# Kernel tuning notes

Measured on AMD Instinct MI355X. Metric: run time of the kernel, lower is better.

The kernel has to match this reference:

```python
import jax, jax.numpy as jnp
import numpy as np

NC = 10          # num_clusters
D_MODEL = 512
H = 8
DK = 64          # d_model = H*DK
B = 8
L = 2048


def _mlp2(x, W1, b1, W2, b2):
    h = jax.nn.gelu(x @ W1 + b1, approximate=False)
    return h @ W2 + b2


def setup_inputs() -> dict:
    key = jax.random.key(0)
    ks = jax.random.split(key, 12)
    s_in = 1.0 / np.sqrt(D_MODEL)
    s_h = 1.0 / np.sqrt(4 * NC)
    s_nc = 1.0 / np.sqrt(NC)
    return {
        "Q": jax.random.normal(ks[0], (B, H, L, DK), jnp.float32),
        "K": jax.random.normal(ks[1], (B, H, L, DK), jnp.float32),
        "V": jax.random.normal(ks[2], (B, H, L, DK), jnp.float32),
        # cluster_k_proj: Linear(d_model,4*nc) GELU Linear(4*nc,nc); stored as [in,out]
        "Wk1": jax.random.normal(ks[3], (D_MODEL, 4 * NC), jnp.float32) * s_in,
        "bk1": jnp.zeros((4 * NC,), jnp.float32),
        "Wk2": jax.random.normal(ks[4], (4 * NC, NC), jnp.float32) * s_h,
        "bk2": jnp.zeros((NC,), jnp.float32),
        # cluster_q_proj
        "Wq1": jax.random.normal(ks[5], (D_MODEL, 4 * NC), jnp.float32) * s_in,
        "bq1": jnp.zeros((4 * NC,), jnp.float32),
        "Wq2": jax.random.normal(ks[6], (4 * NC, NC), jnp.float32) * s_h,
        "bq2": jnp.zeros((NC,), jnp.float32),
        # proj_back_to_cluster_k: Linear(nc, d_model) + GELU
        "Wp": jax.random.normal(ks[7], (NC, D_MODEL), jnp.float32) * s_nc,
        "bp": jnp.zeros((D_MODEL,), jnp.float32),
    }


def _forward(Q, K, V, Wk1, bk1, Wk2, bk2, Wq1, bq1, Wq2, bq2, Wp, bp):
    b, h, l, d_k = Q.shape
    nc = Wk2.shape[1]
    unfolding = 10 * nc

    def pool(x):
        # torch: MaxPool1d(kernel=9, stride=9(default), padding=4) on reshape(b, d_k*h, -1)
        x3 = x.reshape(b, d_k * h, -1)
        y = jax.lax.reduce_window(x3, -jnp.inf, jax.lax.max,
                                  (1, 1, 9), (1, 1, 9),
                                  ((0, 0), (0, 0), (4, 4)))
        return y.reshape(b, h, -1, d_k)

    Kp = pool(K)
    Vp = pool(V)
    l_k = Kp.shape[2]

    # pad along batch dim and take sliding windows of size `unfolding` (stride 1)
    pad = jnp.zeros((unfolding, h, l_k, d_k), Kp.dtype)
    K_padded = jnp.concatenate([pad, Kp[1:]], axis=0)      # [unfolding+b-1, h, l_k, d_k]
    idx = jnp.arange(b)[:, None] + jnp.arange(unfolding)[None, :]
    K_unf = K_padded[idx]                                  # [b, unfolding, h, l_k, d_k]
    K_unf = jnp.transpose(K_unf, (0, 2, 3, 4, 1))          # torch unfold puts window last
    K_unf = K_unf.reshape(b, l_k, unfolding, d_k * h)      # row-major reshape, as torch

    ck = jax.nn.softmax(_mlp2(K_unf, Wk1, bk1, Wk2, bk2), axis=-1)  # [b,l_k,u,nc]
    cq = jax.nn.softmax(_mlp2(K_unf, Wq1, bq1, Wq2, bq2), axis=-1)

    mu = jnp.mean(cq, axis=-1)                             # [b, l_k, unfolding]
    sigma = jax.nn.softplus(jnp.std(cq, axis=-1, ddof=1))  # torch std is unbiased
    x = jnp.mean(ck, axis=-1)
    log_prob = -0.5 * jnp.square((x - mu) / sigma) - jnp.log(sigma) - 0.5 * jnp.log(2.0 * jnp.pi)
    # torch CrossEntropyLoss(mu, mu): classes are dim 1 (l_k), soft prob targets
    logp = jax.nn.log_softmax(mu, axis=1)
    ce = jnp.mean(-jnp.sum(mu * logp, axis=1))
    loss = -jnp.mean(log_prob) + ce

    # fused scatter-style cluster centers: mean over window of cq with assigned cluster zeroed
    assign = jnp.argmax(cq, axis=-1)                       # [b, l_k, unfolding]
    onehot = jax.nn.one_hot(assign, nc, dtype=cq.dtype)    # [b, l_k, u, i] (constant wrt grad)
    total = jnp.sum(cq, axis=2)                            # [b, l_k, nc]
    S = jnp.einsum('blui,bluc->blic', onehot, cq)          # sum of cq at masked positions
    centers = (total[:, :, None, :] - S) / unfolding       # [b, l_k, nc_i, nc_c]
    centers = jnp.transpose(centers, (2, 0, 1, 3))         # [nc, b, l_k, nc]

    cc = jax.nn.gelu(centers @ Wp + bp, approximate=False) # [nc, b, l_k, d_model]
    cc = cc.reshape(b, h, nc, l_k, d_k)                    # faithful torch reshape

    scores = jnp.einsum('bhqd,bhckd->bhqk', Q, cc) / np.sqrt(d_k).astype(Q.dtype)
    attn = jax.nn.softmax(scores, axis=-1)
    context = jnp.einsum('bhqk,bhkd->bhqd', attn, Vp)
    return context, loss


def reference(Q, K, V, Wk1, bk1, Wk2, bk2, Wq1, bq1, Wq2, bq2, Wp, bp):
    return _forward(Q, K, V, Wk1, bk1, Wk2, bk2, Wq1, bq1, Wq2, bq2, Wp, bp)
```

## Files before the change

kernel.cpp:

```cpp
#include <hip/hip_runtime.h>
#include <math.h>

#define NCL 10
#define DM 512
#define NH 8
#define DK 64
#define NB 8
#define SL 2048
#define LK 228
#define UF 100
#define KP_PER_B (NH*LK*DK)
#define KP_TOT (NB*KP_PER_B)
#define NROWS (NB*LK*UF)

typedef __bf16 bf16_t;
typedef __attribute__((ext_vector_type(2))) __bf16 bf16x2;
typedef __attribute__((ext_vector_type(4))) __bf16 bf16x4;
typedef __attribute__((ext_vector_type(8))) __bf16 bf16x8;
typedef __attribute__((ext_vector_type(4))) float f32x4;

__device__ __forceinline__ float gelu_f(float x) {
    return 0.5f * x * (1.f + erff(x * 0.70710678118654752f));
}

__global__ void k_init(float* __restrict__ acc) {
    if (threadIdx.x < 4) acc[threadIdx.x] = 0.f;
}

__global__ void k_prep(const float* __restrict__ Wq1, bf16_t* __restrict__ W1b) {
    int i = blockIdx.x * 256 + threadIdx.x;
    if (i < 512 * 40) W1b[i] = (bf16_t)Wq1[i];
}

__global__ void k_pool(const float* __restrict__ K, const float* __restrict__ V,
                       float* __restrict__ Kp, float* __restrict__ Vp) {
    int idx = blockIdx.x * 256 + threadIdx.x;
    if (idx >= 2 * KP_TOT) return;
    const float* src = (idx < KP_TOT) ? K : V;
    float* dst = (idx < KP_TOT) ? Kp : Vp;
    int e = (idx < KP_TOT) ? idx : idx - KP_TOT;
    int b   = e / KP_PER_B;
    int off = e % KP_PER_B;
    int c  = off / LK;
    int pp = off % LK;
    int p0 = pp * 9 - 4;
    const float* base = src + (size_t)b * 1048576 + (size_t)c * 2048;
    float mx = -3.4e38f;
    #pragma unroll
    for (int j = 0; j < 9; ++j) {
        int p = p0 + j;
        if (p >= 0 && p < 2048) mx = fmaxf(mx, base[p]);
    }
    dst[e] = mx;
}

__global__ __launch_bounds__(256, 6) void k_mlp(
        const float* __restrict__ Kp, const bf16_t* __restrict__ W1b,
        const float* __restrict__ bq1,
        const float* __restrict__ Wq2, const float* __restrict__ bq2,
        float* __restrict__ mu_g, float* __restrict__ centers_g,
        float* __restrict__ acc_g) {
    __shared__ __align__(16) char smem[25040];
    bf16_t* Sst2  = (bf16_t*)smem;
    float*  hT    = (float*)(smem + 8192);
    float*  stats = (float*)(smem + 24592);

    int tid = threadIdx.x;
    int bl = blockIdx.x;
    int b = bl / LK;
    int l = bl % LK;

    for (int s = tid; s < 512 * b; s += 256) {
        int bk = (s >> 9) + 1;
        int rl = s & 511;
        Sst2[(bk << 9) + rl] = (bf16_t)Kp[bk * KP_PER_B + l * 512 + rl];
    }
    if (tid < 111) stats[tid] = 0.f;
    __syncthreads();

    #pragma unroll
    for (int k = 0; k < 4; ++k) {
        int vt = tid + (k << 8);
        if (vt < 1000) {
            int m = vt / 10;
            int n4 = vt - m * 10;
            int base = m << 9;
            float4 h4 = make_float4(0.f, 0.f, 0.f, 0.f);
            for (int s = 1; s <= b; ++s) {
                int t = 99 - b + s;
                int d = (t + 51200 - base) % 100;
                int g = base + d;
                int r = (g - t) / 100;
                const bf16_t* srow = &Sst2[s << 9];
                #pragma unroll 1
                for (; g < base + 512; g += 100, ++r) {
                    float v = (float)srow[r];
                    bf16x4 w = *(const bf16x4*)&W1b[(g - base) * 40 + n4 * 4];
                    h4.x = fmaf(v, (float)w[0], h4.x);
                    h4.y = fmaf(v, (float)w[1], h4.y);
                    h4.z = fmaf(v, (float)w[2], h4.z);
                    h4.w = fmaf(v, (float)w[3], h4.w);
                }
            }
            float* hrow = &hT[m * 41 + n4 * 4];
            hrow[0] = h4.x;
            hrow[1] = h4.y;
            hrow[2] = h4.z;
            hrow[3] = h4.w;
        }
    }
    __syncthreads();

    for (int i = tid; i < 4000; i += 256) {
        int row = i / 40;
        int j = i - row * 40;
        hT[row * 41 + j] = gelu_f(hT[row * 41 + j] + bq1[j]);
    }
    __syncthreads();

    float* total_l = stats;
    float* S_l = stats + 10;
    float* lp_acc = stats + 110;

    if (tid < 100) {
        int row = tid;
        float out[10];
        #pragma unroll
        for (int c = 0; c < 10; ++c) out[c] = bq2[c];
        #pragma unroll
        for (int j = 0; j < 40; ++j) {
            float gj = hT[row * 41 + j];
            #pragma unroll
            for (int c = 0; c < 10; ++c)
                out[c] = fmaf(gj, Wq2[j * 10 + c], out[c]);
        }
        float m = out[0]; int am = 0;
        #pragma unroll
        for (int c = 1; c < 10; ++c)
            if (out[c] > m) { m = out[c]; am = c; }
        float e[10], s = 0.f;
        #pragma unroll
        for (int c = 0; c < 10; ++c) { e[c] = expf(out[c] - m); s += e[c]; }
        float inv = 1.f / s;
        float cq[10], s1 = 0.f;
        #pragma unroll
        for (int c = 0; c < 10; ++c) { cq[c] = e[c] * inv; s1 += cq[c]; }
        float mean = s1 * 0.1f;
        float var = 0.f;
        #pragma unroll
        for (int c = 0; c < 10; ++c) { float d = cq[c] - mean; var += d * d; }
        float sd = sqrtf(var / 9.f);
        float sp = log1pf(expf(sd));
        float lp = -logf(sp) - 0.91893853320467274f;
        mu_g[bl * 100 + row] = mean;
        atomicAdd(lp_acc, lp);
        #pragma unroll
        for (int c = 0; c < 10; ++c) {
            atomicAdd(&total_l[c], cq[c]);
            atomicAdd(&S_l[am * 10 + c], cq[c]);
        }
    }
    __syncthreads();
    if (tid == 0) atomicAdd(&acc_g[0], lp_acc[0]);
    if (tid < 100) {
        centers_g[bl * 100 + tid] = (total_l[tid % 10] - S_l[tid]) * 0.01f;
    }
}

__global__ void k_ce(const float* __restrict__ mu_g, float* __restrict__ acc_g) {
    int bid = blockIdx.x;
    int b = bid / 100;
    int u = bid % 100;
    int lane = threadIdx.x;
    float v[4];
    #pragma unroll
    for (int t = 0; t < 4; ++t) {
        int l = lane + t * 64;
        v[t] = (l < LK) ? mu_g[(b * LK + l) * 100 + u] : -3.4e38f;
    }
    float m = fmaxf(fmaxf(v[0], v[1]), fmaxf(v[2], v[3]));
    for (int o = 32; o > 0; o >>= 1) m = fmaxf(m, __shfl_xor(m, o, 64));
    float se = 0.f;
    #pragma unroll
    for (int t = 0; t < 4; ++t) {
        int l = lane + t * 64;
        if (l < LK) se += expf(v[t] - m);
    }
    for (int o = 32; o > 0; o >>= 1) se += __shfl_xor(se, o, 64);
    float lse = m + logf(se);
    float dot = 0.f;
    #pragma unroll
    for (int t = 0; t < 4; ++t) {
        int l = lane + t * 64;
        if (l < LK) dot += v[t] * (v[t] - lse);
    }
    for (int o = 32; o > 0; o >>= 1) dot += __shfl_xor(dot, o, 64);
    if (lane == 0) atomicAdd(&acc_g[1], -dot * (1.f / 800.f));
}

__global__ void k_ccs(const float* __restrict__ centers_g,
                      const float* __restrict__ Wp, const float* __restrict__ bp,
                      float* __restrict__ ccs) {
    int tid = blockIdx.x * 256 + threadIdx.x;
    if (tid >= KP_TOT) return;
    int k2d2 = tid % (LK * DK);
    int bh = tid / (LK * DK);
    float s = 0.f;
    #pragma unroll
    for (int i2 = 0; i2 < 10; ++i2) {
        int t2 = bh * 145920 + i2 * 14592 + k2d2;
        int i = t2 / 933888;
        int r1 = t2 % 933888;
        int bs = r1 / 116736;
        int r2 = r1 % 116736;
        int ls = r2 / 512;
        int mm = r2 % 512;
        const float* cen = centers_g + (bs * LK + ls) * 100 + i * 10;
        float val = bp[mm];
        #pragma unroll
        for (int c = 0; c < 10; ++c)
            val = fmaf(cen[c], Wp[c * 512 + mm], val);
        s += gelu_f(val);
    }
    ccs[tid] = s;
}

#define QT 128
__global__ __launch_bounds__(256, 3) void k_attn(
        const float* __restrict__ Q, const float* __restrict__ ccs,
        const float* __restrict__ Vp, float* __restrict__ outp) {
    __shared__ __align__(16) char smem[36864];
    bf16_t* Kl = (bf16_t*)(smem);
    bf16_t* Vt = (bf16_t*)(smem + 9216);
    bf16_t* Pl = (bf16_t*)(smem + 18432);

    int tid = threadIdx.x;
    int wid = tid >> 6;
    int lane = tid & 63;
    int ln = lane & 15;
    int qd = lane >> 4;
    int bid = blockIdx.x;
    int bh = bid >> 4;
    int qt = bid & 15;
    int qbase = qt * QT;

    const float* Qbh = Q + (size_t)bh * SL * DK;
    const float* Kbh = ccs + (size_t)bh * LK * DK;
    const float* Vbh = Vp + (size_t)bh * LK * DK;

    for (int s = tid; s < QT * 32; s += 256) {
        int r = s >> 5;
        int c2 = s & 31;
        float2 v = *(const float2*)&Qbh[(size_t)(qbase + r) * DK + c2 * 2];
        *(bf16x2*)&Pl[r * 72 + c2 * 2] = (bf16x2){(bf16_t)v.x, (bf16_t)v.y};
    }
    __syncthreads();
    bf16x8 qf[2][2];
    #pragma unroll
    for (int mt = 0; mt < 2; ++mt)
        #pragma unroll
        for (int ks = 0; ks < 2; ++ks)
            qf[mt][ks] = *(const bf16x8*)&Pl[(wid * 32 + mt * 16 + ln) * 72 + ks * 32 + qd * 8];

    f32x4 acc_o[2][4];
    float mrow[2][4], lrow[2][4];
    #pragma unroll
    for (int mt = 0; mt < 2; ++mt)
        #pragma unroll
        for (int t = 0; t < 4; ++t) {
            acc_o[mt][t] = (f32x4)(0.f);
            mrow[mt][t] = -3.0e38f;
            lrow[mt][t] = 0.f;
        }

    for (int ch = 0; ch < 4; ++ch) {
        int k0 = ch * 64;
        __syncthreads();
        for (int s = tid; s < 64 * 32; s += 256) {
            int kk = s >> 5;
            int c2 = s & 31;
            int key = k0 + kk;
            float2 v = (key < LK) ? *(const float2*)&Kbh[(size_t)key * DK + c2 * 2]
                                  : make_float2(0.f, 0.f);
            *(bf16x2*)&Kl[kk * 72 + c2 * 2] = (bf16x2){(bf16_t)v.x, (bf16_t)v.y};
        }
        for (int s = tid; s < 64 * 16; s += 256) {
            int kk = s >> 4;
            int c4 = s & 15;
            int key = k0 + kk;
            float4 v = (key < LK) ? *(const float4*)&Vbh[(size_t)key * DK + c4 * 4]
                                  : make_float4(0.f, 0.f, 0.f, 0.f);
            Vt[(c4 * 4 + 0) * 72 + kk] = (bf16_t)v.x;
            Vt[(c4 * 4 + 1) * 72 + kk] = (bf16_t)v.y;
            Vt[(c4 * 4 + 2) * 72 + kk] = (bf16_t)v.z;
            Vt[(c4 * 4 + 3) * 72 + kk] = (bf16_t)v.w;
        }
        __syncthreads();

        f32x4 accs[2][4];
        #pragma unroll
        for (int mt = 0; mt < 2; ++mt)
            #pragma unroll
            for (int nt = 0; nt < 4; ++nt) accs[mt][nt] = (f32x4)(0.f);
        #pragma unroll
        for (int ks = 0; ks < 2; ++ks) {
            #pragma unroll
            for (int nt = 0; nt < 4; ++nt) {
                bf16x8 bf = *(const bf16x8*)&Kl[(nt * 16 + ln) * 72 + ks * 32 + qd * 8];
                #pragma unroll
                for (int mt = 0; mt < 2; ++mt)
                    accs[mt][nt] = __builtin_amdgcn_mfma_f32_16x16x32_bf16(qf[mt][ks], bf, accs[mt][nt], 0, 0, 0);
            }
        }

        #pragma unroll
        for (int mt = 0; mt < 2; ++mt) {
            #pragma unroll
            for (int r = 0; r < 4; ++r) {
                float sv[4];
                #pragma unroll
                for (int nt = 0; nt < 4; ++nt) {
                    float s = accs[mt][nt][r] * 0.125f;
                    int key = k0 + nt * 16 + ln;
                    sv[nt] = (key < LK) ? s : -3.0e38f;
                }
                float rmax = fmaxf(fmaxf(sv[0], sv[1]), fmaxf(sv[2], sv[3]));
                #pragma unroll
                for (int o = 1; o < 16; o <<= 1)
                    rmax = fmaxf(rmax, __shfl_xor(rmax, o, 64));
                float mold = mrow[mt][r];
                float mnew = fmaxf(mold, rmax);
                float alpha = __expf(mold - mnew);
                float p[4], psum = 0.f;
                #pragma unroll
                for (int nt = 0; nt < 4; ++nt) {
                    p[nt] = __expf(sv[nt] - mnew);
                    psum += p[nt];
                }
                #pragma unroll
                for (int o = 1; o < 16; o <<= 1)
                    psum += __shfl_xor(psum, o, 64);
                lrow[mt][r] = lrow[mt][r] * alpha + psum;
                mrow[mt][r] = mnew;
                #pragma unroll
                for (int ntv = 0; ntv < 4; ++ntv)
                    acc_o[mt][ntv][r] *= alpha;
                int prow = (wid * 32 + mt * 16 + qd * 4 + r) * 72;
                #pragma unroll
                for (int nt = 0; nt < 4; ++nt)
                    Pl[prow + nt * 16 + ln] = (bf16_t)p[nt];
            }
        }

        #pragma unroll
        for (int ks = 0; ks < 2; ++ks) {
            bf16x8 pa[2];
            #pragma unroll
            for (int mt = 0; mt < 2; ++mt)
                pa[mt] = *(const bf16x8*)&Pl[(wid * 32 + mt * 16 + ln) * 72 + ks * 32 + qd * 8];
            #pragma unroll
            for (int ntv = 0; ntv < 4; ++ntv) {
                bf16x8 vb = *(const bf16x8*)&Vt[(ntv * 16 + ln) * 72 + ks * 32 + qd * 8];
                #pragma unroll
                for (int mt = 0; mt < 2; ++mt)
                    acc_o[mt][ntv] = __builtin_amdgcn_mfma_f32_16x16x32_bf16(pa[mt], vb, acc_o[mt][ntv], 0, 0, 0);
            }
        }
    }

    #pragma unroll
    for (int mt = 0; mt < 2; ++mt) {
        #pragma unroll
        for (int r = 0; r < 4; ++r) {
            float inv = 1.f / lrow[mt][r];
            int q_idx = qbase + wid * 32 + mt * 16 + qd * 4 + r;
            float* orow = outp + ((size_t)bh * SL + q_idx) * DK;
            #pragma unroll
            for (int ntv = 0; ntv < 4; ++ntv)
                orow[ntv * 16 + ln] = acc_o[mt][ntv][r] * inv;
        }
    }
}

__global__ void k_final(const float* __restrict__ acc_g, float* __restrict__ outp) {
    outp[8388608] = -(acc_g[0] * (1.f / (float)NROWS)) + acc_g[1];
}

extern "C" void kernel_launch(void* const* d_in, const int* in_sizes, int n_in,
                              void* d_out, int out_size, void* d_ws, size_t ws_size,
                              hipStream_t stream) {
    const float* Q   = (const float*)d_in[0];
    const float* K   = (const float*)d_in[1];
    const float* V   = (const float*)d_in[2];
    const float* Wq1 = (const float*)d_in[7];
    const float* bq1 = (const float*)d_in[8];
    const float* Wq2 = (const float*)d_in[9];
    const float* bq2 = (const float*)d_in[10];
    const float* Wp  = (const float*)d_in[11];
    const float* bp  = (const float*)d_in[12];
    float* out = (float*)d_out;

    float* ws      = (float*)d_ws;
    float* Kp      = ws;
    float* Vp      = ws + 933888;
    float* mu      = ws + 1867776;
    float* centers = ws + 2050176;
    float* ccs     = ws + 2232576;
    float* acc     = ws + 3166464;
    bf16_t* W1b    = (bf16_t*)(ws + 3166468);

    k_init<<<1, 64, 0, stream>>>(acc);
    k_prep<<<80, 256, 0, stream>>>(Wq1, W1b);
    k_pool<<<(2 * KP_TOT + 255) / 256, 256, 0, stream>>>(K, V, Kp, Vp);
    k_mlp<<<NB * LK, 256, 0, stream>>>(Kp, W1b, bq1, Wq2, bq2, mu, centers, acc);
    k_ce<<<NB * 100, 64, 0, stream>>>(mu, acc);
    k_ccs<<<(KP_TOT + 255) / 256, 256, 0, stream>>>(centers, Wp, bp, ccs);
    k_attn<<<NB * NH * (SL / QT), 256, 0, stream>>>(Q, ccs, Vp, out);
    k_final<<<1, 1, 0, stream>>>(acc, out);
}
```

Before: 364.3 us.

## Fuse small prep kernels into pool, specialize MLP layer1 by batch, finalize via last-block

Folds the init and weight-conversion kernels into the pooling launch as extra blocks, and moves the final loss write into the CE kernel using an atomic last-block counter. This removes three tiny launches. The MLP first layer is rewritten as a per-batch template with fixed trip counts, 8-wide bf16 weight loads and fp32 staging of the pooled keys. The hidden-activation stride becomes 44 so rows can be read as float4. Occupancy drops because the launch bound goes from 6 to 4 blocks per unit and shared memory use grows.

```diff
diff --git a/kernel.cpp b/kernel.cpp
--- a/kernel.cpp
+++ b/kernel.cpp
@@ -12,10 +12,10 @@
 #define KP_PER_B (NH*LK*DK)
 #define KP_TOT (NB*KP_PER_B)
 #define NROWS (NB*LK*UF)
+#define POOL_BLOCKS 7296
 
 typedef __bf16 bf16_t;
 typedef __attribute__((ext_vector_type(2))) __bf16 bf16x2;
-typedef __attribute__((ext_vector_type(4))) __bf16 bf16x4;
 typedef __attribute__((ext_vector_type(8))) __bf16 bf16x8;
 typedef __attribute__((ext_vector_type(4))) float f32x4;
 
@@ -23,19 +23,18 @@
     return 0.5f * x * (1.f + erff(x * 0.70710678118654752f));
 }
 
-__global__ void k_init(float* __restrict__ acc) {
-    if (threadIdx.x < 4) acc[threadIdx.x] = 0.f;
-}
-
-__global__ void k_prep(const float* __restrict__ Wq1, bf16_t* __restrict__ W1b) {
-    int i = blockIdx.x * 256 + threadIdx.x;
-    if (i < 512 * 40) W1b[i] = (bf16_t)Wq1[i];
-}
-
 __global__ void k_pool(const float* __restrict__ K, const float* __restrict__ V,
-                       float* __restrict__ Kp, float* __restrict__ Vp) {
-    int idx = blockIdx.x * 256 + threadIdx.x;
-    if (idx >= 2 * KP_TOT) return;
+                       float* __restrict__ Kp, float* __restrict__ Vp,
+                       const float* __restrict__ Wq1, bf16_t* __restrict__ W1b,
+                       float* __restrict__ acc) {
+    int bid = blockIdx.x;
+    if (bid >= POOL_BLOCKS) {
+        int i = (bid - POOL_BLOCKS) * 256 + threadIdx.x;
+        if (i < 512 * 40) W1b[i] = (bf16_t)Wq1[i];
+        if (bid == POOL_BLOCKS && threadIdx.x < 4) acc[threadIdx.x] = 0.f;
+        return;
+    }
+    int idx = bid * 256 + threadIdx.x;
     const float* src = (idx < KP_TOT) ? K : V;
     float* dst = (idx < KP_TOT) ? Kp : Vp;
     int e = (idx < KP_TOT) ? idx : idx - KP_TOT;
@@ -54,67 +53,88 @@
     dst[e] = mx;
 }
 
-__global__ __launch_bounds__(256, 6) void k_mlp(
+template<int B>
+__device__ __forceinline__ void layer1(int tid, const bf16_t* __restrict__ W1b,
+                                       const float* __restrict__ Sstf,
+                                       float* __restrict__ hT) {
+    #pragma unroll 1
+    for (int k = 0; k < 2; ++k) {
+        int vt = tid + (k << 8);
+        if (vt < 500) {
+            int m = vt / 5;
+            int h8 = vt - m * 5;
+            int bm = (12 * m) % 100;
+            float h[8];
+            #pragma unroll
+            for (int i = 0; i < 8; ++i) h[i] = 0.f;
+            #pragma unroll
+            for (int s = 1; s <= B; ++s) {
+                const int t = 99 - B + s;
+                int d0 = t - bm; if (d0 < 0) d0 += 100;
+                int r0 = ((m << 9) + d0 - t) / 100;
+                const float* srow = &Sstf[s << 9];
+                #pragma unroll
+                for (int j = 0; j < 6; ++j) {
+                    int c = d0 + j * 100;
+                    if (j < 5 || c < 512) {
+                        float v = srow[r0 + j];
+                        bf16x8 w = *(const bf16x8*)&W1b[c * 40 + h8 * 8];
+                        #pragma unroll
+                        for (int i = 0; i < 8; ++i)
+                            h[i] = fmaf(v, (float)w[i], h[i]);
+                    }
+                }
+            }
+            #pragma unroll
+            for (int i = 0; i < 8; ++i) hT[m * 44 + h8 * 8 + i] = h[i];
+        }
+    }
+}
+
+__global__ __launch_bounds__(256, 4) void k_mlp(
         const float* __restrict__ Kp, const bf16_t* __restrict__ W1b,
         const float* __restrict__ bq1,
         const float* __restrict__ Wq2, const float* __restrict__ bq2,
         float* __restrict__ mu_g, float* __restrict__ centers_g,
         float* __restrict__ acc_g) {
-    __shared__ __align__(16) char smem[25040];
-    bf16_t* Sst2  = (bf16_t*)smem;
-    float*  hT    = (float*)(smem + 8192);
-    float*  stats = (float*)(smem + 24592);
+    __shared__ __align__(16) char smem[34432];
+    float* Sstf  = (float*)smem;
+    float* hT    = (float*)(smem + 16384);
+    float* stats = (float*)(smem + 33984);
 
     int tid = threadIdx.x;
     int bl = blockIdx.x;
     int b = bl / LK;
     int l = bl % LK;
 
-    for (int s = tid; s < 512 * b; s += 256) {
-        int bk = (s >> 9) + 1;
-        int rl = s & 511;
-        Sst2[(bk << 9) + rl] = (bf16_t)Kp[bk * KP_PER_B + l * 512 + rl];
+    for (int s4 = tid; s4 < 128 * b; s4 += 256) {
+        int bk = (s4 >> 7) + 1;
+        int r4 = (s4 & 127) << 2;
+        *(float4*)&Sstf[(bk << 9) + r4] =
+            *(const float4*)&Kp[bk * KP_PER_B + l * 512 + r4];
     }
     if (tid < 111) stats[tid] = 0.f;
+    if (b == 0) {
+        for (int i = tid; i < 4400; i += 256) hT[i] = 0.f;
+    }
     __syncthreads();
 
-    #pragma unroll
-    for (int k = 0; k < 4; ++k) {
-        int vt = tid + (k << 8);
-        if (vt < 1000) {
-            int m = vt / 10;
-            int n4 = vt - m * 10;
-            int base = m << 9;
-            float4 h4 = make_float4(0.f, 0.f, 0.f, 0.f);
-            for (int s = 1; s <= b; ++s) {
-                int t = 99 - b + s;
-                int d = (t + 51200 - base) % 100;
-                int g = base + d;
-                int r = (g - t) / 100;
-                const bf16_t* srow = &Sst2[s << 9];
-                #pragma unroll 1
-                for (; g < base + 512; g += 100, ++r) {
-                    float v = (float)srow[r];
-                    bf16x4 w = *(const bf16x4*)&W1b[(g - base) * 40 + n4 * 4];
-                    h4.x = fmaf(v, (float)w[0], h4.x);
-                    h4.y = fmaf(v, (float)w[1], h4.y);
-                    h4.z = fmaf(v, (float)w[2], h4.z);
-                    h4.w = fmaf(v, (float)w[3], h4.w);
-                }
-            }
-            float* hrow = &hT[m * 41 + n4 * 4];
-            hrow[0] = h4.x;
-            hrow[1] = h4.y;
-            hrow[2] = h4.z;
-            hrow[3] = h4.w;
-        }
+    switch (b) {
+        case 1: layer1<1>(tid, W1b, Sstf, hT); break;
+        case 2: layer1<2>(tid, W1b, Sstf, hT); break;
+        case 3: layer1<3>(tid, W1b, Sstf, hT); break;
+        case 4: layer1<4>(tid, W1b, Sstf, hT); break;
+        case 5: layer1<5>(tid, W1b, Sstf, hT); break;
+        case 6: layer1<6>(tid, W1b, Sstf, hT); break;
+        case 7: layer1<7>(tid, W1b, Sstf, hT); break;
+        default: break;
     }
     __syncthreads();
 
     for (int i = tid; i < 4000; i += 256) {
         int row = i / 40;
         int j = i - row * 40;
-        hT[row * 41 + j] = gelu_f(hT[row * 41 + j] + bq1[j]);
+        hT[row * 44 + j] = gelu_f(hT[row * 44 + j] + bq1[j]);
     }
     __syncthreads();
 
@@ -124,12 +144,19 @@
 
     if (tid < 100) {
         int row = tid;
+        float g[40];
+        #pragma unroll
+        for (int j4 = 0; j4 < 10; ++j4) {
+            float4 gv = *(const float4*)&hT[row * 44 + j4 * 4];
+            g[j4 * 4 + 0] = gv.x; g[j4 * 4 + 1] = gv.y;
+            g[j4 * 4 + 2] = gv.z; g[j4 * 4 + 3] = gv.w;
+        }
         float out[10];
         #pragma unroll
         for (int c = 0; c < 10; ++c) out[c] = bq2[c];
         #pragma unroll
         for (int j = 0; j < 40; ++j) {
-            float gj = hT[row * 41 + j];
+            float gj = g[j];
             #pragma unroll
             for (int c = 0; c < 10; ++c)
                 out[c] = fmaf(gj, Wq2[j * 10 + c], out[c]);
@@ -167,7 +194,8 @@
     }
 }
 
-__global__ void k_ce(const float* __restrict__ mu_g, float* __restrict__ acc_g) {
+__global__ void k_ce(const float* __restrict__ mu_g, float* __restrict__ acc_g,
+                     float* __restrict__ outp) {
     int bid = blockIdx.x;
     int b = bid / 100;
     int u = bid % 100;
@@ -195,7 +223,15 @@
         if (l < LK) dot += v[t] * (v[t] - lse);
     }
     for (int o = 32; o > 0; o >>= 1) dot += __shfl_xor(dot, o, 64);
-    if (lane == 0) atomicAdd(&acc_g[1], -dot * (1.f / 800.f));
+    if (lane == 0) {
+        atomicAdd(&acc_g[1], -dot * (1.f / 800.f));
+        __threadfence();
+        unsigned int old = atomicAdd((unsigned int*)&acc_g[2], 1u);
+        if (old == 799u) {
+            __threadfence();
+            outp[8388608] = -(acc_g[0] * (1.f / (float)NROWS)) + acc_g[1];
+        }
+    }
 }
 
 __global__ void k_ccs(const float* __restrict__ centers_g,
@@ -380,10 +416,6 @@
                 orow[ntv * 16 + ln] = acc_o[mt][ntv][r] * inv;
         }
     }
-}
-
-__global__ void k_final(const float* __restrict__ acc_g, float* __restrict__ outp) {
-    outp[8388608] = -(acc_g[0] * (1.f / (float)NROWS)) + acc_g[1];
 }
 
 extern "C" void kernel_launch(void* const* d_in, const int* in_sizes, int n_in,
@@ -409,12 +441,9 @@
     float* acc     = ws + 3166464;
     bf16_t* W1b    = (bf16_t*)(ws + 3166468);
 
-    k_init<<<1, 64, 0, stream>>>(acc);
-    k_prep<<<80, 256, 0, stream>>>(Wq1, W1b);
-    k_pool<<<(2 * KP_TOT + 255) / 256, 256, 0, stream>>>(K, V, Kp, Vp);
+    k_pool<<<POOL_BLOCKS + 80, 256, 0, stream>>>(K, V, Kp, Vp, Wq1, W1b, acc);
     k_mlp<<<NB * LK, 256, 0, stream>>>(Kp, W1b, bq1, Wq2, bq2, mu, centers, acc);
-    k_ce<<<NB * 100, 64, 0, stream>>>(mu, acc);
     k_ccs<<<(KP_TOT + 255) / 256, 256, 0, stream>>>(centers, Wp, bp, ccs);
+    k_ce<<<NB * 100, 64, 0, stream>>>(mu, acc, out);
     k_attn<<<NB * NH * (SL / QT), 256, 0, stream>>>(Q, ccs, Vp, out);
-    k_final<<<1, 1, 0, stream>>>(acc, out);
-}
+}
```

Result: faster. 348.3 us (-4.4%).
